# Kernel tuning notes

Measured on AMD Instinct MI355X. Metric: run time of the kernel, lower is better.

The kernel has to match this reference:

```python
import jax, jax.numpy as jnp
import numpy as np

B, TT, T, L, V, E, H = 16, 8, 64, 100, 32000, 512, 512
EO = 2 * H          # encoder output size == decoder hidden size
A = 512             # attention size
IN = E + EO + E     # decoder raw input size
TEMP = IN // 2      # sharp_linear output size
sg = jax.lax.stop_gradient


def _lstm_cell(x, h, c, Wih, Whh, bih, bhh):
    # PyTorch LSTM gate order: i, f, g, o
    g = x @ Wih.T + bih + h @ Whh.T + bhh
    i, f, gg, o = jnp.split(g, 4, axis=-1)
    c = jax.nn.sigmoid(f) * c + jax.nn.sigmoid(i) * jnp.tanh(gg)
    h = jax.nn.sigmoid(o) * jnp.tanh(c)
    return h, c


def setup_inputs():
    key = jax.random.key(0)
    ks = jax.random.split(key, 24)
    s = 0.05
    rn = lambda k, sh: jax.random.normal(k, sh, jnp.float32) * s
    z = lambda *sh: jnp.zeros(sh, jnp.float32)
    return {
        "embedding": rn(ks[0], (V, E)),
        "enc_Wih_f": rn(ks[1], (4 * H, E)), "enc_Whh_f": rn(ks[2], (4 * H, H)),
        "enc_bih_f": z(4 * H), "enc_bhh_f": z(4 * H),
        "enc_Wih_b": rn(ks[3], (4 * H, E)), "enc_Whh_b": rn(ks[4], (4 * H, H)),
        "enc_bih_b": z(4 * H), "enc_bhh_b": z(4 * H),
        "W1": rn(ks[5], (A, EO)), "W2": rn(ks[6], (A, EO)),
        "mem_W": rn(ks[7], (E, EO)), "mem_b": z(E),
        "U1": rn(ks[8], (E, E)), "V1": rn(ks[9], (E, E)),
        "U2": rn(ks[10], (E, E)), "V2": rn(ks[11], (E, E)),
        "sharp_W": rn(ks[12], (TEMP, IN)), "sharp_b": z(TEMP),
        "dec_Wih": rn(ks[13], (4 * EO, TEMP)), "dec_Whh": rn(ks[14], (4 * EO, EO)),
        "dec_bih": z(4 * EO), "dec_bhh": z(4 * EO),
        "fc_W": rn(ks[15], (V, EO)), "fc_b": z(V),
        "topic": jax.random.randint(ks[16], (B, TT), 0, V),
        "topic_len": jnp.full((B,), TT, jnp.int32),
        "essay_input": jax.random.randint(ks[17], (B, T), 0, V),
        "essay_len": jnp.full((B,), T, jnp.int32),
        "mems": jax.random.randint(ks[18], (B, L), 0, V),
    }


def reference(embedding, enc_Wih_f, enc_Whh_f, enc_bih_f, enc_bhh_f,
              enc_Wih_b, enc_Whh_b, enc_bih_b, enc_bhh_b,
              W1, W2, mem_W, mem_b, U1, V1, U2, V2,
              sharp_W, sharp_b, dec_Wih, dec_Whh, dec_bih, dec_bhh,
              fc_W, fc_b, topic, topic_len, essay_input, essay_len, mems):
    Bsz = topic.shape[0]
    Tlen = essay_input.shape[1]

    # ---------------- Encoder (1-layer bidirectional LSTM) ----------------
    # all topic_len equal -> pack/sort is identity
    x = embedding[topic].transpose(1, 0, 2)  # [TT, B, E]

    def mk_cell(Wih, Whh, bih, bhh):
        def f(carry, xt):
            h, c = carry
            h, c = _lstm_cell(xt, h, c, Wih, Whh, bih, bhh)
            return (h, c), h
        return f

    z0 = (jnp.zeros((Bsz, H), x.dtype), jnp.zeros((Bsz, H), x.dtype))
    (hf, cf), outs_f = jax.lax.scan(mk_cell(enc_Wih_f, enc_Whh_f, enc_bih_f, enc_bhh_f), z0, x)
    (hb, cb), outs_b = jax.lax.scan(mk_cell(enc_Wih_b, enc_Whh_b, enc_bih_b, enc_bhh_b), z0, x[::-1])
    outs_b = outs_b[::-1]
    topics = jnp.concatenate([outs_f, outs_b], axis=-1).transpose(1, 0, 2)  # [B, TT, 2H]
    h = jnp.concatenate([hf, hb], axis=-1)  # [B, EO]
    c = jnp.concatenate([cf, cb], axis=-1)  # [B, EO]

    # ---------------- external memory ----------------
    M = embedding[mems]                      # [B, L, E]
    pre_t = topics @ W1.T                    # [B, TT, A]  (precompute attention keys)

    def update_memory(M, emb):
        # all reads of stored memory are detached in the original module
        Md = sg(M)
        e = emb[:, None, :]                  # [B, 1, E]
        Mt = jnp.tanh(Md @ U1.T + e @ V1.T)
        gate = jax.nn.sigmoid(Md @ U2.T + e @ V2.T)
        Mn = gate * Mt + (1.0 - gate) * Md
        return jnp.where(jnp.isfinite(Mn), Mn, jnp.float32(1e-31))

    def before_feed(emb, h_last, c_last, M):
        # topic attention (query = decoder cell state)
        q = c_last @ W2.T                                       # [B, A]
        alpha = jax.nn.softmax(jnp.einsum('bta,ba->bt', pre_t, q), axis=1)
        c_t = jnp.einsum('btd,bt->bd', topics, alpha)           # [B, EO]
        # content-addressed memory read (query = decoder hidden)
        v = jnp.tanh(h_last @ mem_W.T + mem_b)                  # [B, E]
        Md = sg(M)
        qm = jax.nn.softmax(jnp.einsum('ble,be->bl', Md, v), axis=1)
        m_t = jnp.einsum('bl,ble->be', qm, Md)                  # [B, E]
        return jnp.concatenate([emb, c_t, m_t], axis=1)         # [B, IN]

    # ---------------- decode (teacher forcing) ----------------
    emb0 = embedding[essay_input[:, 0]]
    M = update_memory(M, emb0)
    dec_in = before_feed(emb0, h, c, M)

    # steps 1..T-1 feed essay_input[:, t]; last scan step's memory update is unused
    toks = jnp.concatenate([essay_input[:, 1:], essay_input[:, -1:]], axis=1).T  # [T, B]

    def step(carry, tok):
        h, c, M, dec_in = carry
        xs = dec_in @ sharp_W.T + sharp_b
        h, c = _lstm_cell(xs, h, c, dec_Wih, dec_Whh, dec_bih, dec_bhh)
        logits = h @ fc_W.T + fc_b                              # [B, V]
        emb = embedding[tok]
        M = update_memory(M, emb)
        dec_in = before_feed(emb, h, c, M)
        return (h, c, M, dec_in), logits

    _, logits = jax.lax.scan(step, (h, c, M, dec_in), toks)
    return logits.transpose(1, 0, 2)  # [B, T, V]
```

## Files before the change

kernel.cpp:

```cpp
#include <hip/hip_runtime.h>
#include <math.h>

#define DEVI __device__ __forceinline__

typedef unsigned short us8 __attribute__((ext_vector_type(8)));
typedef short bfv __attribute__((ext_vector_type(8)));
typedef float f32x4 __attribute__((ext_vector_type(4)));

DEVI float sigmf_(float x){ return 1.0f/(1.0f+expf(-x)); }
DEVI float dot4_(const float4 a, const float4 b){ return a.x*b.x + a.y*b.y + a.z*b.z + a.w*b.w; }
DEVI float wred64(float v){
#pragma unroll
  for (int m = 32; m; m >>= 1) v += __shfl_xor(v, m);
  return v;
}
DEVI float b2f(unsigned short u){ return __uint_as_float(((unsigned)u)<<16); }
DEVI unsigned short f2bf(float x){
  unsigned u = __float_as_uint(x);
  return (unsigned short)((u + 0x7FFFu + ((u>>16)&1u)) >> 16);
}
DEVI void f2bf2(float x, unsigned short& hi, unsigned short& lo){
  hi = f2bf(x);
  lo = f2bf(x - b2f(hi));
}
// ... 60 lines not shown
}

__global__ void pack_k(const float* __restrict__ U1, const float* __restrict__ U2,
                       const float* __restrict__ sharpW,
                       float* __restrict__ UcatI, float* __restrict__ Ws3T)
{
  int gid = blockIdx.x*256 + threadIdx.x;
  if (gid < 524288){
    int n = gid>>9, k = gid&511;
    UcatI[gid] = (n&1) ? U2[(size_t)(n>>1)*512+k] : U1[(size_t)(n>>1)*512+k];
  } else {
    int g2 = gid - 524288;
    int k = g2>>10, j = g2&1023;
    Ws3T[g2] = sharpW[(size_t)j*2048 + 1536 + k];
  }
}

__global__ void pack_u_hilo(const float* __restrict__ U1, const float* __restrict__ U2,
                            unsigned short* __restrict__ Uhi, unsigned short* __restrict__ Ulo)
{
  int gid = blockIdx.x*256 + threadIdx.x;
  int n = gid>>9, k = gid&511;
  float v = (n&1) ? U2[(size_t)(n>>1)*512+k] : U1[(size_t)(n>>1)*512+k];
  unsigned short h, l;
  f2bf2(v, h, l);
  Uhi[gid] = h; Ulo[gid] = l;
}

__global__ void pack_ws3b(const float* __restrict__ sharpW,
                          unsigned short* __restrict__ hi, unsigned short* __restrict__ lo)
{
  int gid = blockIdx.x*256 + threadIdx.x;
  int j = gid>>9, k = gid&511;
  float v = sharpW[(size_t)j*2048 + 1536 + k];
  unsigned short h, l;
  f2bf2(v, h, l);
  hi[gid] = h; lo[gid] = l;
}

__global__ void conv_k(const float* __restrict__ src, unsigned short* __restrict__ dst, int n8){
  int i = blockIdx.x*256 + threadIdx.x;
  if (i >= n8) return;
  float4 a = ((const float4*)src)[2*i], b = ((const float4*)src)[2*i+1];
  us8 o;
  o[0]=f2bf(a.x); o[1]=f2bf(a.y); o[2]=f2bf(a.z); o[3]=f2bf(a.w);
  o[4]=f2bf(b.x); o[5]=f2bf(b.y); o[6]=f2bf(b.z); o[7]=f2bf(b.w);
  ((us8*)dst)[i] = o;
}

__global__ void conv2_k(const float* __restrict__ src,
                        unsigned short* __restrict__ hi, unsigned short* __restrict__ lo, int n8){
  int i = blockIdx.x*256 + threadIdx.x;
  if (i >= n8) return;
  float4 a = ((const float4*)src)[2*i], b = ((const float4*)src)[2*i+1];
  us8 oh, ol;
  oh[0]=f2bf(a.x); ol[0]=f2bf_lo(a.x, oh[0]);
  oh[1]=f2bf(a.y); ol[1]=f2bf_lo(a.y, oh[1]);
  oh[2]=f2bf(a.z); ol[2]=f2bf_lo(a.z, oh[2]);
  oh[3]=f2bf(a.w); ol[3]=f2bf_lo(a.w, oh[3]);
  oh[4]=f2bf(b.x); ol[4]=f2bf_lo(b.x, oh[4]);
  oh[5]=f2bf(b.y); ol[5]=f2bf_lo(b.y, oh[5]);
  oh[6]=f2bf(b.z); ol[6]=f2bf_lo(b.z, oh[6]);
  oh[7]=f2bf(b.w); ol[7]=f2bf_lo(b.w, oh[7]);
  ((us8*)hi)[i] = oh;
  ((us8*)lo)[i] = ol;
}

template<int ACT>
__global__ void gemm_nt(const float* __restrict__ A, int lda,
                        const float* __restrict__ W, int ldw, int woff,
                        const float* __restrict__ bias,
                        float* __restrict__ C, int ldc, int M, int N, int K)
{
  __shared__ float As[1024], Ws[1024];
  const int bm = blockIdx.y*64, bn = blockIdx.x*64;
  const int tid = threadIdx.x;
  const int lr = tid>>2, lk = (tid&3)<<2;
  const int tm = (tid>>4)<<2, tn = (tid&15)<<2;
  float acc[4][4] = {};
  for (int k0 = 0; k0 < K; k0 += 16){
    float4 av = make_float4(0.f,0.f,0.f,0.f);
    if (bm+lr < M) av = *(const float4*)(A + (size_t)(bm+lr)*lda + k0 + lk);
    As[(lk+0)*64+lr]=av.x; As[(lk+1)*64+lr]=av.y; As[(lk+2)*64+lr]=av.z; As[(lk+3)*64+lr]=av.w;
    float4 wv = make_float4(0.f,0.f,0.f,0.f);
    if (bn+lr < N) wv = *(const float4*)(W + (size_t)(bn+lr)*ldw + woff + k0 + lk);
    Ws[(lk+0)*64+lr]=wv.x; Ws[(lk+1)*64+lr]=wv.y; Ws[(lk+2)*64+lr]=wv.z; Ws[(lk+3)*64+lr]=wv.w;
    __syncthreads();
#pragma unroll
    for (int k = 0; k < 16; ++k){
      float4 a = *(const float4*)&As[k*64+tm];
      float4 w = *(const float4*)&Ws[k*64+tn];
      acc[0][0]+=a.x*w.x; acc[0][1]+=a.x*w.y; acc[0][2]+=a.x*w.z; acc[0][3]+=a.x*w.w;
      acc[1][0]+=a.y*w.x; acc[1][1]+=a.y*w.y; acc[1][2]+=a.y*w.z; acc[1][3]+=a.y*w.w;
      acc[2][0]+=a.z*w.x; acc[2][1]+=a.z*w.y; acc[2][2]+=a.z*w.z; acc[2][3]+=a.z*w.w;
      acc[3][0]+=a.w*w.x; acc[3][1]+=a.w*w.y; acc[3][2]+=a.w*w.z; acc[3][3]+=a.w*w.w;
    }
    __syncthreads();
  }
#pragma unroll
  for (int i = 0; i < 4; ++i){
    int m = bm+tm+i; if (m >= M) continue;
#pragma unroll
    for (int j = 0; j < 4; ++j){
      int n = bn+tn+j; if (n >= N) continue;
      float v = acc[i][j] + (bias ? bias[n] : 0.f);
      if (ACT == 1) v = tanhf(v);
      C[(size_t)m*ldc + n] = v;
    }
  }
}

__global__ void enc_step(const float* __restrict__ xtop,
    const float* __restrict__ Wih_f, const float* __restrict__ Whh_f,
    const float* __restrict__ bih_f, const float* __restrict__ bhh_f,
    const float* __restrict__ Wih_b, const float* __restrict__ Whh_b,
    const float* __restrict__ bih_b, const float* __restrict__ bhh_b,
    const float* __restrict__ h_in, const float* __restrict__ c_in,
    float* __restrict__ h_out, float* __restrict__ c_out,
    float* __restrict__ topics, int t)
{
  const int dir = blockIdx.y;
  const int j = blockIdx.x*4 + (threadIdx.x>>6);
  const int lane = threadIdx.x & 63;
  const int b = lane & 15, g4 = lane >> 4;
  const int tt = dir ? (7 - t) : t;
  const float* Wih = dir ? Wih_b : Wih_f;
  const float* Whh = dir ? Whh_b : Whh_f;
  const float* bih = dir ? bih_b : bih_f;
  const float* bhh = dir ? bhh_b : bhh_f;
  const int row = g4*512 + j;
  float acc = bih[row] + bhh[row];
  const float4* wx = (const float4*)(Wih + (size_t)row*512);
  const float4* xv = (const float4*)(xtop + (size_t)(tt*16+b)*512);
#pragma unroll 8
  for (int k = 0; k < 128; ++k) acc += dot4_(wx[k], xv[k]);
  const float4* wh = (const float4*)(Whh + (size_t)row*512);
  const float4* hv = (const float4*)(h_in + (size_t)b*1024 + dir*512);
#pragma unroll 8
  for (int k = 0; k < 128; ++k) acc += dot4_(wh[k], hv[k]);
  float gi = __shfl(acc, b);
  float gf = __shfl(acc, b+16);
  float gg = __shfl(acc, b+32);
  float go = __shfl(acc, b+48);
  if (g4 == 0){
    float c_old = c_in[(size_t)b*1024 + dir*512 + j];
    float cn = sigmf_(gf)*c_old + sigmf_(gi)*tanhf(gg);
    float hn = sigmf_(go)*tanhf(cn);
    h_out[(size_t)b*1024 + dir*512 + j] = hn;
    c_out[(size_t)b*1024 + dir*512 + j] = cn;
    topics[(size_t)(b*8+tt)*1024 + dir*512 + j] = hn;
  }
}

DEVI void mem_gemm_role(int bid, const float* __restrict__ Min, float* __restrict__ Mout,
                        const float* __restrict__ U,
                        const float* __restrict__ eV1s, const float* __restrict__ eV2s,
                        float* lds, int tid)
{
  const int bm = (bid>>4)*64, bn = (bid&15)*64;
  float* As = lds; float* Ws = lds + 1024;
  const int lr = tid>>2, lk = (tid&3)<<2;
  const int tm = (tid>>4)<<2, tn = (tid&15)<<2;
  float acc[4][4] = {};
  for (int k0 = 0; k0 < 512; k0 += 16){
    float4 av = *(const float4*)(Min + (size_t)(bm+lr)*512 + k0 + lk);
    As[(lk+0)*64+lr]=av.x; As[(lk+1)*64+lr]=av.y; As[(lk+2)*64+lr]=av.z; As[(lk+3)*64+lr]=av.w;
    float4 wv = *(const float4*)(U + (size_t)(bn+lr)*512 + k0 + lk);
    Ws[(lk+0)*64+lr]=wv.x; Ws[(lk+1)*64+lr]=wv.y; Ws[(lk+2)*64+lr]=wv.z; Ws[(lk+3)*64+lr]=wv.w;
    __syncthreads();
#pragma unroll
    for (int k = 0; k < 16; ++k){
      float4 a = *(const float4*)&As[k*64+tm];
      float4 w = *(const float4*)&Ws[k*64+tn];
      acc[0][0]+=a.x*w.x; acc[0][1]+=a.x*w.y; acc[0][2]+=a.x*w.z; acc[0][3]+=a.x*w.w;
      acc[1][0]+=a.y*w.x; acc[1][1]+=a.y*w.y; acc[1][2]+=a.y*w.z; acc[1][3]+=a.y*w.w;
      acc[2][0]+=a.z*w.x; acc[2][1]+=a.z*w.y; acc[2][2]+=a.z*w.z; acc[2][3]+=a.z*w.w;
      acc[3][0]+=a.w*w.x; acc[3][1]+=a.w*w.y; acc[3][2]+=a.w*w.z; acc[3][3]+=a.w*w.w;
    }
    __syncthreads();
  }
  const int e0 = (bn+tn)>>1;
#pragma unroll
  for (int i = 0; i < 4; ++i){
    int r = bm+tm+i;
    int b = r/100;
#pragma unroll
    for (int p = 0; p < 2; ++p){
      int e = e0 + p;
      float oldv = Min[(size_t)r*512 + e];
      float mt = tanhf (acc[i][2*p]   + eV1s[(size_t)b*512 + e]);
      float g  = sigmf_(acc[i][2*p+1] + eV2s[(size_t)b*512 + e]);
      float mn = g*mt + (1.f-g)*oldv;
      if (!isfinite(mn)) mn = 1e-31f;
      Mout[(size_t)r*512 + e] = mn;
    }
  }
}

__global__ void mem_update_k(const float* __restrict__ Min, float* __restrict__ Mout,
                             const float* __restrict__ U,
                             const float* __restrict__ eV1s, const float* __restrict__ eV2s)
{
  __shared__ float lds[2080];
  mem_gemm_role(blockIdx.x, Min, Mout, U, eV1s, eV2s, lds, threadIdx.x);
}

DEVI void mem_ep(f32x4 v, int m0, int n0, int i, int j, int kg, int r16, int lane,
                 const float* __restrict__ Min,
                 const float* __restrict__ eV1s, const float* __restrict__ eV2s,
                 float* __restrict__ Mout,
                 unsigned short* __restrict__ Mohi, unsigned short* __restrict__ Molo)
{
#pragma unroll
  for (int q = 0; q < 4; ++q){
    float val = v[q];
    float oth = __shfl_xor(val, 1);
    if (!(lane&1)){
      int m = m0 + i*16 + kg*4 + q;
      int n = n0 + j*16 + r16;
      int e = n>>1, bb = m/100;
      float mold = Min[(size_t)m*512 + e];
      float mt = tanhf (val + eV1s[(size_t)bb*512 + e]);
      float g  = sigmf_(oth + eV2s[(size_t)bb*512 + e]);
      float mn = g*mt + (1.f-g)*mold;
      if (!isfinite(mn)) mn = 1e-31f;
      Mout[(size_t)m*512 + e] = mn;
      unsigned short h, l;
      f2bf2(mn, h, l);
      Mohi[(size_t)m*512 + e] = h;
      Molo[(size_t)m*512 + e] = l;
    }
  }
}

DEVI void mem_mfma_role2(int hwbid, const float* __restrict__ Min,
                        const unsigned short* __restrict__ Mhi, const unsigned short* __restrict__ Mlo,
                        float* __restrict__ Mout,
                        unsigned short* __restrict__ Mohi, unsigned short* __restrict__ Molo,
                        const unsigned short* __restrict__ Uhi, const unsigned short* __restrict__ Ulo,
                        const float* __restrict__ eV1s, const float* __restrict__ eV2s,
                        int tid, float* __restrict__ lds)
{
  const int bid2 = (hwbid & 7)*200 + (hwbid >> 3);
  const int bm = (bid2 >> 5)*32, bn = (bid2 & 31)*32;
  const int wave = tid>>6, lane = tid&63;
  const int r16 = lane&15, kg = lane>>4;
  const size_t aoff = (size_t)(bm + r16)*512 + wave*128 + kg*8;
  const size_t boff = (size_t)(bn + r16)*512 + wave*128 + kg*8;
  const unsigned short* pa0h = Mhi + aoff; const unsigned short* pa0l = Mlo + aoff;
  const unsigned short* pb0h = Uhi + boff; const unsigned short* pb0l = Ulo + boff;
  f32x4 c00 = {}, c01 = {}, c10 = {}, c11 = {};
#pragma unroll
  for (int k0 = 0; k0 < 128; k0 += 32){
    bfv a0h = *(const bfv*)(pa0h + k0);
    bfv a0l = *(const bfv*)(pa0l + k0);
    bfv a1h = *(const bfv*)(pa0h + 16*512 + k0);
    bfv a1l = *(const bfv*)(pa0l + 16*512 + k0);
    bfv b0h = *(const bfv*)(pb0h + k0);
    bfv b0l = *(const bfv*)(pb0l + k0);
    bfv b1h = *(const bfv*)(pb0h + 16*512 + k0);
    bfv b1l = *(const bfv*)(pb0l + 16*512 + k0);
    c00 = __builtin_amdgcn_mfma_f32_16x16x32_bf16(a0h, b0h, c00, 0, 0, 0);
    c00 = __builtin_amdgcn_mfma_f32_16x16x32_bf16(a0h, b0l, c00, 0, 0, 0);
    c00 = __builtin_amdgcn_mfma_f32_16x16x32_bf16(a0l, b0h, c00, 0, 0, 0);
    c01 = __builtin_amdgcn_mfma_f32_16x16x32_bf16(a0h, b1h, c01, 0, 0, 0);
    c01 = __builtin_amdgcn_mfma_f32_16x16x32_bf16(a0h, b1l, c01, 0, 0, 0);
    c01 = __builtin_amdgcn_mfma_f32_16x16x32_bf16(a0l, b1h, c01, 0, 0, 0);
    c10 = __builtin_amdgcn_mfma_f32_16x16x32_bf16(a1h, b0h, c10, 0, 0, 0);
    c10 = __builtin_amdgcn_mfma_f32_16x16x32_bf16(a1h, b0l, c10, 0, 0, 0);
    c10 = __builtin_amdgcn_mfma_f32_16x16x32_bf16(a1l, b0h, c10, 0, 0, 0);
    c11 = __builtin_amdgcn_mfma_f32_16x16x32_bf16(a1h, b1h, c11, 0, 0, 0);
    c11 = __builtin_amdgcn_mfma_f32_16x16x32_bf16(a1h, b1l, c11, 0, 0, 0);
    c11 = __builtin_amdgcn_mfma_f32_16x16x32_bf16(a1l, b1h, c11, 0, 0, 0);
  }
  float* wbase = lds + wave*1024 + lane*4;
#pragma unroll
  for (int q = 0; q < 4; ++q){
    wbase[q]     = c00[q];
    wbase[256+q] = c01[q];
    wbase[512+q] = c10[q];
    wbase[768+q] = c11[q];
  }
  __syncthreads();
  f32x4 s;
#pragma unroll
  for (int q = 0; q < 4; ++q)
    s[q] = lds[       wave*256 + lane*4 + q] + lds[1024 + wave*256 + lane*4 + q]
         + lds[2048 + wave*256 + lane*4 + q] + lds[3072 + wave*256 + lane*4 + q];
  mem_ep(s, bm, bn, wave>>1, wave&1, kg, r16, lane, Min, eV1s, eV2s, Mout, Mohi, Molo);
}

__global__ __launch_bounds__(256,4) void mem_update_k2(
    const float* __restrict__ Min,
    const unsigned short* __restrict__ Mhi, const unsigned short* __restrict__ Mlo,
    float* __restrict__ Mout,
    unsigned short* __restrict__ Mohi, unsigned short* __restrict__ Molo,
    const unsigned short* __restrict__ Uhi, const unsigned short* __restrict__ Ulo,
    const float* __restrict__ eV1s, const float* __restrict__ eV2s)
{
  __shared__ float lds[4096];
  mem_mfma_role2(blockIdx.x, Min, Mhi, Mlo, Mout, Mohi, Molo, Uhi, Ulo, eV1s, eV2s, threadIdx.x, lds);
}

__global__ void step_pre(const float* __restrict__ Min, float* __restrict__ Mout,
    const float* __restrict__ U,
    const float* __restrict__ eV1s, const float* __restrict__ eV2s,
    const float* __restrict__ qb, const float* __restrict__ vb,
    const float* __restrict__ pret, const float* __restrict__ tws2,
    const float* __restrict__ eWs1t, const float* __restrict__ sharp_b,
    const float* __restrict__ Ws3T, float* __restrict__ xs)
{
  __shared__ float lds[2080];
  const int tid = threadIdx.x;
  if (blockIdx.x >= 16){
    mem_gemm_role(blockIdx.x-16, Min, Mout, U, eV1s, eV2s, lds, tid);
    return;
  }
  const int b = blockIdx.x;
  lds[tid]         = qb[b*512 + tid];
  lds[tid+256]     = qb[b*512 + tid + 256];
  lds[512+tid]     = vb[b*512 + tid];
  lds[512+tid+256] = vb[b*512 + tid + 256];
  __syncthreads();
  {
    const int tq = tid>>5, l32 = tid&31;
    const float* pr = pret + (size_t)(b*8+tq)*512;
    float sv = 0.f;
#pragma unroll
    for (int i = 0; i < 16; ++i){ int a = l32 + 32*i; sv += pr[a]*lds[a]; }
#pragma unroll
    for (int m = 16; m; m >>= 1) sv += __shfl_xor(sv, m);
    if (l32 == 0) lds[1024+tq] = sv;
  }
  __syncthreads();
  {
    float mx = -1e30f;
#pragma unroll
    for (int i = 0; i < 8; ++i) mx = fmaxf(mx, lds[1024+i]);
    float sm = 0.f; float ev[8];
#pragma unroll
    for (int i = 0; i < 8; ++i){ ev[i] = expf(lds[1024+i]-mx); sm += ev[i]; }
    if (tid < 8) lds[1032+tid] = ev[tid]/sm;
  }
  __syncthreads();
  {
    const int wv = tid>>6, lane = tid&63;
    for (int l = wv; l < 100; l += 4){
      const float* Mr = Min + (size_t)(b*100+l)*512;
      float sv = 0.f;
#pragma unroll
      for (int i = 0; i < 8; ++i){ int k = lane + 64*i; sv += Mr[k]*lds[512+k]; }
      sv = wred64(sv);
      if (lane == 0) lds[1040+l] = sv;
    }
  }
  __syncthreads();
  float mx = -1e30f;
  for (int i = 0; i < 100; ++i) mx = fmaxf(mx, lds[1040+i]);
  __syncthreads();
  if (tid < 100) lds[1040+tid] = expf(lds[1040+tid]-mx);
  __syncthreads();
  float sm = 0.f;
  for (int i = 0; i < 100; ++i) sm += lds[1040+i];
  const float inv = 1.f/sm;
  for (int e = tid; e < 512; e += 256){
    float a = 0.f;
    for (int l = 0; l < 100; ++l) a += lds[1040+l]*Min[(size_t)(b*100+l)*512 + e];
    lds[1152+e] = a*inv;
  }
  __syncthreads();
  float a0[4];
#pragma unroll
  for (int r2 = 0; r2 < 4; ++r2){
    int j = tid + 256*r2;
    float v = sharp_b[j] + eWs1t[(size_t)b*1024 + j];
#pragma unroll
    for (int t2 = 0; t2 < 8; ++t2) v += lds[1032+t2]*tws2[(size_t)(b*8+t2)*1024 + j];
    a0[r2] = v;
  }
  for (int k = 0; k < 512; ++k){
    float mk = lds[1152+k];
    const float* wr = Ws3T + (size_t)k*1024;
    a0[0] += mk*wr[tid];
    a0[1] += mk*wr[tid+256];
    a0[2] += mk*wr[tid+512];
    a0[3] += mk*wr[tid+768];
  }
#pragma unroll
  for (int r2 = 0; r2 < 4; ++r2) xs[(size_t)b*1024 + tid + 256*r2] = a0[r2];
}

__global__ __launch_bounds__(256,4) void attn_mt(
    const float* __restrict__ Min,
    const unsigned short* __restrict__ Mhi, const unsigned short* __restrict__ Mlo,
    float* __restrict__ Mout,
    unsigned short* __restrict__ Mohi, unsigned short* __restrict__ Molo,
    const unsigned short* __restrict__ Uhi, const unsigned short* __restrict__ Ulo,
    const float* __restrict__ eV1s, const float* __restrict__ eV2s,
    const float* __restrict__ qb, const float* __restrict__ vb,
    const float* __restrict__ pret,
    float* __restrict__ alphab,
    unsigned short* __restrict__ mthi, unsigned short* __restrict__ mtlo)
{
  __shared__ float lds[4096];
  const int tid = threadIdx.x;
  if (blockIdx.x >= 128){
    mem_mfma_role2(blockIdx.x-128, Min, Mhi, Mlo, Mout, Mohi, Molo, Uhi, Ulo, eV1s, eV2s, tid, lds);
    return;
  }
  const int b = blockIdx.x >> 3, ec = blockIdx.x & 7;
  lds[tid]         = qb[b*512 + tid];
  lds[tid+256]     = qb[b*512 + tid + 256];
  lds[512+tid]     = vb[b*512 + tid];
  lds[512+tid+256] = vb[b*512 + tid + 256];
  __syncthreads();
  if (ec == 0){
    {
      const int tq = tid>>5, l32 = tid&31;
      const float* pr = pret + (size_t)(b*8+tq)*512;
      float sv = 0.f;
#pragma unroll
      for (int i = 0; i < 16; ++i){ int a = l32 + 32*i; sv += pr[a]*lds[a]; }
#pragma unroll
      for (int m = 16; m; m >>= 1) sv += __shfl_xor(sv, m);
      if (l32 == 0) lds[1024+tq] = sv;
    }
    __syncthreads();
    {
      float mx = -1e30f;
#pragma unroll
      for (int i = 0; i < 8; ++i) mx = fmaxf(mx, lds[1024+i]);
      float sm = 0.f; float ev[8];
#pragma unroll
      for (int i = 0; i < 8; ++i){ ev[i] = expf(lds[1024+i]-mx); sm += ev[i]; }
      if (tid < 8) alphab[b*8+tid] = ev[tid]/sm;
    }
    __syncthreads();
  }
  {
    const int wv = tid>>6, lane = tid&63;
    for (int l = wv; l < 100; l += 4){
      const float* Mr = Min + (size_t)(b*100+l)*512;
      float sv = 0.f;
#pragma unroll
      for (int i = 0; i < 8; ++i){ int k = lane + 64*i; sv += Mr[k]*lds[512+k]; }
      sv = wred64(sv);
      if (lane == 0) lds[1040+l] = sv;
    }
  }
  __syncthreads();
  {
    const int wv = tid>>6;
    float v100 = (tid < 100) ? lds[1040+tid] : -1e30f;
    float m1 = v100;
#pragma unroll
    for (int m = 32; m; m >>= 1) m1 = fmaxf(m1, __shfl_xor(m1, m));
    if ((tid&63) == 0) lds[1664+wv] = m1;
    __syncthreads();
    float mx = fmaxf(fmaxf(lds[1664], lds[1665]), fmaxf(lds[1666], lds[1667]));
    float e = (tid < 100) ? expf(v100 - mx) : 0.f;
    float s1 = e;
#pragma unroll
    for (int m = 32; m; m >>= 1) s1 += __shfl_xor(s1, m);
    if ((tid&63) == 0) lds[1668+wv] = s1;
    __syncthreads();
    float sm = lds[1668]+lds[1669]+lds[1670]+lds[1671];
    if (tid < 100) lds[1800+tid] = e/sm;
  }
  __syncthreads();
  {
    const int e = ec*64 + (tid & 63);
    const int lg = tid >> 6;
    float a = 0.f;
    for (int l = lg*25; l < lg*25 + 25; ++l)
      a += lds[1800+l] * Min[(size_t)(b*100 + l)*512 + e];
    lds[1904 + lg*64 + (tid & 63)] = a;
    __syncthreads();
    if (lg == 0){
      float s = lds[1904 + tid] + lds[1968 + tid] + lds[2032 + tid] + lds[2096 + tid];
      unsigned short h, l2;
      f2bf2(s, h, l2);
      mthi[b*512 + e] = h;
      mtlo[b*512 + e] = l2;
    }
  }
}

__global__ __launch_bounds__(256) void xs_k(
    const unsigned short* __restrict__ Ws3hi, const unsigned short* __restrict__ Ws3lo,
    const unsigned short* __restrict__ mthi, const unsigned short* __restrict__ mtlo,
    const float* __restrict__ alphab, const float* __restrict__ sharp_b,
    const float* __restrict__ eWs1t, const float* __restrict__ tws2,
    unsigned short* __restrict__ xshi, unsigned short* __restrict__ xslo)
{
  __shared__ float lds[1024];
  const int tid = threadIdx.x, wave = tid>>6, lane = tid&63;
  const int r16 = lane&15, kg = lane>>4;
  const int jt = blockIdx.x;
  const size_t aoff = (size_t)(jt*16 + r16)*512 + wave*128 + kg*8;
  const size_t boff = (size_t)r16*512 + wave*128 + kg*8;
  f32x4 c0 = {};
#pragma unroll
  for (int k0 = 0; k0 < 128; k0 += 32){
    bfv ah = *(const bfv*)(Ws3hi + aoff + k0);
    bfv al = *(const bfv*)(Ws3lo + aoff + k0);
    bfv bh = *(const bfv*)(mthi + boff + k0);
    bfv bl = *(const bfv*)(mtlo + boff + k0);
    c0 = __builtin_amdgcn_mfma_f32_16x16x32_bf16(ah, bh, c0, 0,0,0);
    c0 = __builtin_amdgcn_mfma_f32_16x16x32_bf16(ah, bl, c0, 0,0,0);
    c0 = __builtin_amdgcn_mfma_f32_16x16x32_bf16(al, bh, c0, 0,0,0);
  }
  float* wb2 = lds + wave*256 + lane*4;
#pragma unroll
  for (int q = 0; q < 4; ++q) wb2[q] = c0[q];
  __syncthreads();
  if (wave == 0){
    const int b = r16;
#pragma unroll
    for (int q = 0; q < 4; ++q){
      float s = lds[lane*4+q] + lds[256+lane*4+q] + lds[512+lane*4+q] + lds[768+lane*4+q];
      int j = jt*16 + kg*4 + q;
      float v2 = s + sharp_b[j] + eWs1t[(size_t)b*1024 + j];
#pragma unroll
      for (int t2 = 0; t2 < 8; ++t2) v2 += alphab[b*8+t2]*tws2[(size_t)(b*8+t2)*1024 + j];
      unsigned short h, l;
      f2bf2(v2, h, l);
      xshi[b*1024+j] = h;
      xslo[b*1024+j] = l;
    }
  }
}

__global__ void dec_lstm(const float* __restrict__ xs,
    const float* __restrict__ Wih, const float* __restrict__ Whh,
    const float* __restrict__ bih, const float* __restrict__ bhh,
    const float* __restrict__ h_in, const float* __restrict__ c_in,
    float* __restrict__ h_out, float* __restrict__ c_out)
{
  const int j = blockIdx.x*4 + (threadIdx.x>>6);
  const int lane = threadIdx.x & 63;
  const int b = lane & 15, g4 = lane >> 4;
  const int row = g4*1024 + j;
  float acc = bih[row] + bhh[row];
  const float4* w1 = (const float4*)(Wih + (size_t)row*1024);
  const float4* x1 = (const float4*)(xs + (size_t)b*1024);
#pragma unroll 8
  for (int k = 0; k < 256; ++k) acc += dot4_(w1[k], x1[k]);
  const float4* w2 = (const float4*)(Whh + (size_t)row*1024);
  const float4* h1 = (const float4*)(h_in + (size_t)b*1024);
#pragma unroll 8
  for (int k = 0; k < 256; ++k) acc += dot4_(w2[k], h1[k]);
  float gi = __shfl(acc, b);
  float gf = __shfl(acc, b+16);
  float gg = __shfl(acc, b+32);
  float go = __shfl(acc, b+48);
  if (g4 == 0){
    float c_old = c_in[(size_t)b*1024 + j];
    float cn = sigmf_(gf)*c_old + sigmf_(gi)*tanhf(gg);
    float hn = sigmf_(go)*tanhf(cn);
    h_out[(size_t)b*1024 + j] = hn;
    c_out[(size_t)b*1024 + j] = cn;
  }
}

__global__ __launch_bounds__(256) void dec_mfma(
    const unsigned short* __restrict__ xsh, const unsigned short* __restrict__ xsl,
    const unsigned short* __restrict__ Wih_h, const unsigned short* __restrict__ Wih_l,
    const unsigned short* __restrict__ Whh_h, const unsigned short* __restrict__ Whh_l,
    const float* __restrict__ bih, const float* __restrict__ bhh,
    const unsigned short* __restrict__ hih, const unsigned short* __restrict__ hil,
    const float* __restrict__ c_in,
    float* __restrict__ h_out, float* __restrict__ c_out,
    unsigned short* __restrict__ hoh, unsigned short* __restrict__ hol,
    unsigned short* __restrict__ coh, unsigned short* __restrict__ col_)
{
  __shared__ float acc_lds[4][4][64][4];
  __shared__ float gat[4][64][4];
  const int tid = threadIdx.x, kh = tid>>6, lane = tid&63;
  const int r16 = lane&15, kg = lane>>4;
  const int jt = blockIdx.x;
  const size_t arow = (size_t)(jt*16 + r16)*1024 + kh*256 + kg*8;
  const size_t boff = (size_t)r16*1024 + kh*256 + kg*8;
  f32x4 c0 = {}, c1 = {}, c2 = {}, c3 = {};
#pragma unroll 2
  for (int k0 = 0; k0 < 256; k0 += 32){
    bfv bxh = *(const bfv*)(xsh + boff + k0);
    bfv bxl = *(const bfv*)(xsl + boff + k0);
    bfv bhh_ = *(const bfv*)(hih + boff + k0);
    bfv bhl_ = *(const bfv*)(hil + boff + k0);
#define DEC_GATE(G, CC) { \
    bfv aih = *(const bfv*)(Wih_h + arow + (size_t)(G)*1048576 + k0); \
    bfv ail = *(const bfv*)(Wih_l + arow + (size_t)(G)*1048576 + k0); \
    bfv ahh = *(const bfv*)(Whh_h + arow + (size_t)(G)*1048576 + k0); \
    bfv ahl = *(const bfv*)(Whh_l + arow + (size_t)(G)*1048576 + k0); \
    CC = __builtin_amdgcn_mfma_f32_16x16x32_bf16(aih, bxh, CC, 0,0,0); \
    CC = __builtin_amdgcn_mfma_f32_16x16x32_bf16(aih, bxl, CC, 0,0,0); \
    CC = __builtin_amdgcn_mfma_f32_16x16x32_bf16(ail, bxh, CC, 0,0,0); \
    CC = __builtin_amdgcn_mfma_f32_16x16x32_bf16(ahh, bhh_, CC, 0,0,0); \
    CC = __builtin_amdgcn_mfma_f32_16x16x32_bf16(ahh, bhl_, CC, 0,0,0); \
    CC = __builtin_amdgcn_mfma_f32_16x16x32_bf16(ahl, bhh_, CC, 0,0,0); }
    DEC_GATE(0, c0)
    DEC_GATE(1, c1)
    DEC_GATE(2, c2)
    DEC_GATE(3, c3)
#undef DEC_GATE
  }
#pragma unroll
  for (int q = 0; q < 4; ++q){
    acc_lds[kh][0][lane][q] = c0[q];
    acc_lds[kh][1][lane][q] = c1[q];
    acc_lds[kh][2][lane][q] = c2[q];
    acc_lds[kh][3][lane][q] = c3[q];
  }
  __syncthreads();
  {
    const int g = kh;
#pragma unroll
    for (int q = 0; q < 4; ++q)
      gat[g][lane][q] = acc_lds[0][g][lane][q] + acc_lds[1][g][lane][q]
                      + acc_lds[2][g][lane][q] + acc_lds[3][g][lane][q];
  }
  __syncthreads();
  {
    const int b = tid&15, joff = tid>>4;
    const int l2 = (joff>>2)*16 + b, q2 = joff&3;
    const int j = jt*16 + joff;
    float gi = gat[0][l2][q2] + bih[j]        + bhh[j];
    float gf = gat[1][l2][q2] + bih[1024+j]   + bhh[1024+j];
    float gg = gat[2][l2][q2] + bih[2048+j]   + bhh[2048+j];
    float go = gat[3][l2][q2] + bih[3072+j]   + bhh[3072+j];
    float cold = c_in[b*1024 + j];
    float cn = sigmf_(gf)*cold + sigmf_(gi)*tanhf(gg);
    float hn = sigmf_(go)*tanhf(cn);
    h_out[b*1024 + j] = hn;
    c_out[b*1024 + j] = cn;
    unsigned short uh, ul;
    f2bf2(hn, uh, ul); hoh[b*1024+j] = uh; hol[b*1024+j] = ul;
    f2bf2(cn, uh, ul); coh[b*1024+j] = uh; col_[b*1024+j] = ul;
  }
}

template<typename WT>
__global__ __launch_bounds__(256,4) void step_out_t(const float* __restrict__ h, const float* __restrict__ c,
    const WT* __restrict__ fcW_, const float* __restrict__ fcb,
    const float* __restrict__ W2, const float* __restrict__ memW,
    const float* __restrict__ memb,
    float* __restrict__ out, float* __restrict__ qb, float* __restrict__ vb, int t)
{
  __shared__ float tile[256];
  const int bid = blockIdx.x;
  const int wv = threadIdx.x>>6, lane = threadIdx.x&63;
  const int b = lane&15, jj = lane>>4;
  if (bid < 2000){
    const int j = bid*16 + wv*4 + jj;
    float acc = kdot1024(fcW_ + (size_t)j*1024, (const float4*)(h + (size_t)b*1024));
    tile[(wv*4+jj)*16 + b] = acc;
    __syncthreads();
    const int b2 = threadIdx.x>>4, j2 = threadIdx.x&15;
    out[(size_t)b2*2048000 + (size_t)t*32000 + bid*16 + j2] = tile[j2*16+b2] + fcb[bid*16+j2];
  } else if (bid < 2032){
    const int j = (bid-2000)*16 + wv*4 + jj;
    float acc = kdot1024(W2 + (size_t)j*1024, (const float4*)(c + (size_t)b*1024));
    qb[b*512 + j] = acc;
  } else {
    const int j = (bid-2032)*16 + wv*4 + jj;
    float acc = kdot1024(memW + (size_t)j*1024, (const float4*)(h + (size_t)b*1024));
    vb[b*512 + j] = tanhf(acc + memb[j]);
  }
}

__global__ __launch_bounds__(256) void step_out_m(
    const unsigned short* __restrict__ fcWb, const float* __restrict__ fcb,
    const unsigned short* __restrict__ W2h, const unsigned short* __restrict__ W2l,
    const unsigned short* __restrict__ mWh, const unsigned short* __restrict__ mWl,
    const float* __restrict__ memb,
    const unsigned short* __restrict__ hh, const unsigned short* __restrict__ hl,
    const unsigned short* __restrict__ ch, const unsigned short* __restrict__ cl,
    float* __restrict__ out, float* __restrict__ qb, float* __restrict__ vb, int t)
{
  const int tid = threadIdx.x, wave = tid>>6, lane = tid&63;
  const int r16 = lane&15, kg = lane>>4;
  const int bid = blockIdx.x;
  const size_t boff = (size_t)r16*1024 + kg*8;
  if (bid < 500){
    const int tile = bid*4 + wave;
    const unsigned short* pa0 = fcWb + (size_t)(tile*16 + r16)*1024 + kg*8;
    const unsigned short* pbh = hh + boff;
    const unsigned short* pbl = hl + boff;
    f32x4 c0 = {};
#pragma unroll 4
    for (int k0 = 0; k0 < 1024; k0 += 32){
      bfv a0 = *(const bfv*)(pa0 + k0);
      bfv b0 = *(const bfv*)(pbh + k0);
      bfv b1 = *(const bfv*)(pbl + k0);
      c0 = __builtin_amdgcn_mfma_f32_16x16x32_bf16(a0, b0, c0, 0,0,0);
      c0 = __builtin_amdgcn_mfma_f32_16x16x32_bf16(a0, b1, c0, 0,0,0);
    }
    float* ob = out + (size_t)r16*2048000 + (size_t)t*32000;
#pragma unroll
    for (int q = 0; q < 4; ++q){
      int j0 = tile*16 + kg*4 + q;
      ob[j0] = c0[q] + fcb[j0];
    }
  } else if (bid < 508){
    const int tile = (bid-500)*4 + wave;
    const unsigned short* pah = W2h + (size_t)(tile*16 + r16)*1024 + kg*8;
    const unsigned short* pal = W2l + (size_t)(tile*16 + r16)*1024 + kg*8;
    const unsigned short* pbh = ch + boff;
    const unsigned short* pbl = cl + boff;
    f32x4 c0 = {};
#pragma unroll 4
    for (int k0 = 0; k0 < 1024; k0 += 32){
      bfv ah = *(const bfv*)(pah + k0);
      bfv al = *(const bfv*)(pal + k0);
      bfv b0 = *(const bfv*)(pbh + k0);
      bfv b1 = *(const bfv*)(pbl + k0);
      c0 = __builtin_amdgcn_mfma_f32_16x16x32_bf16(ah, b0, c0, 0,0,0);
      c0 = __builtin_amdgcn_mfma_f32_16x16x32_bf16(ah, b1, c0, 0,0,0);
      c0 = __builtin_amdgcn_mfma_f32_16x16x32_bf16(al, b0, c0, 0,0,0);
    }
#pragma unroll
    for (int q = 0; q < 4; ++q)
      qb[r16*512 + tile*16 + kg*4 + q] = c0[q];
  } else {
    const int tile = (bid-508)*4 + wave;
    const unsigned short* pah = mWh + (size_t)(tile*16 + r16)*1024 + kg*8;
    const unsigned short* pal = mWl + (size_t)(tile*16 + r16)*1024 + kg*8;
    const unsigned short* pbh = hh + boff;
    const unsigned short* pbl = hl + boff;
    f32x4 c0 = {};
#pragma unroll 4
    for (int k0 = 0; k0 < 1024; k0 += 32){
      bfv ah = *(const bfv*)(pah + k0);
      bfv al = *(const bfv*)(pal + k0);
      bfv b0 = *(const bfv*)(pbh + k0);
      bfv b1 = *(const bfv*)(pbl + k0);
      c0 = __builtin_amdgcn_mfma_f32_16x16x32_bf16(ah, b0, c0, 0,0,0);
      c0 = __builtin_amdgcn_mfma_f32_16x16x32_bf16(ah, b1, c0, 0,0,0);
      c0 = __builtin_amdgcn_mfma_f32_16x16x32_bf16(al, b0, c0, 0,0,0);
    }
#pragma unroll
    for (int q = 0; q < 4; ++q){
      int j = tile*16 + kg*4 + q;
      vb[r16*512 + j] = tanhf(c0[q] + memb[j]);
    }
  }
}

extern "C" void kernel_launch(void* const* d_in, const int* in_sizes, int n_in,
                              void* d_out, int out_size, void* d_ws, size_t ws_size,
                              hipStream_t stream)
{
  const float* embedding = (const float*)d_in[0];
  const float* Wih_f = (const float*)d_in[1];
  const float* Whh_f = (const float*)d_in[2];
  const float* bih_f = (const float*)d_in[3];
  const float* bhh_f = (const float*)d_in[4];
  const float* Wih_b = (const float*)d_in[5];
  const float* Whh_b = (const float*)d_in[6];
  const float* bih_b = (const float*)d_in[7];
  const float* bhh_b = (const float*)d_in[8];
  const float* W1    = (const float*)d_in[9];
  const float* W2    = (const float*)d_in[10];
  const float* mem_W = (const float*)d_in[11];
  const float* mem_b = (const float*)d_in[12];
  const float* U1    = (const float*)d_in[13];
  const float* V1    = (const float*)d_in[14];
  const float* U2    = (const float*)d_in[15];
  const float* V2    = (const float*)d_in[16];
  const float* sharp_W = (const float*)d_in[17];
  const float* sharp_b = (const float*)d_in[18];
  const float* dec_Wih = (const float*)d_in[19];
  const float* dec_Whh = (const float*)d_in[20];
  const float* dec_bih = (const float*)d_in[21];
  const float* dec_bhh = (const float*)d_in[22];
  const float* fc_W  = (const float*)d_in[23];
  const float* fc_b  = (const float*)d_in[24];
  const int* topic   = (const int*)d_in[25];
  const int* essay   = (const int*)d_in[27];
  const int* mems    = (const int*)d_in[29];
  float* out = (float*)d_out;
  float* ws = (float*)d_ws;

  float* x_topic = ws;
  float* embs    = ws + 65536;
  float* eV1     = ws + 598016;
  float* eV2     = ws + 1130496;
  float* eWs1    = ws + 1662976;
  float* topics  = ws + 2727936;
  float* tws2    = ws + 2859008;
  float* pret    = ws + 2990080;
  float* Mb0     = ws + 3055616;
  float* Mb1     = ws + 3874816;
  float* h_buf   = ws + 4694016;
  float* c_buf   = ws + 4726784;
  float* xs      = ws + 4759552;
  float* qb      = ws + 4775936;
  float* vb      = ws + 4784128;
  float* UcatI   = ws + 4792320;
  float* Ws3T    = ws + 5316608;
  unsigned short* Ws3hi = (unsigned short*)(ws + 4792320);
  unsigned short* Ws3lo = (unsigned short*)(ws + 5054464);
  unsigned short* mthi  = (unsigned short*)(ws + 5316608);
  unsigned short* mtlo  = (unsigned short*)(ws + 5320704);
  float*          alphab= ws + 5324800;
  unsigned short* Uhi   = (unsigned short*)(ws + 5840896);
  unsigned short* Ulo   = (unsigned short*)(ws + 6103040);
  unsigned short* Mb0hi = (unsigned short*)(ws + 6365184);
  unsigned short* Mb0lo = (unsigned short*)(ws + 6774784);
  unsigned short* Mb1hi = (unsigned short*)(ws + 7184384);
  unsigned short* Mb1lo = (unsigned short*)(ws + 7593984);
  unsigned short* fcWb  = (unsigned short*)(ws + 8003584);
  unsigned short* dWihHi = (unsigned short*)(ws + 24387584);
  unsigned short* dWihLo = (unsigned short*)(ws + 26484736);
  unsigned short* dWhhHi = (unsigned short*)(ws + 28581888);
  unsigned short* dWhhLo = (unsigned short*)(ws + 30679040);
  unsigned short* W2h    = (unsigned short*)(ws + 32776192);
  unsigned short* W2l    = (unsigned short*)(ws + 33038336);
  unsigned short* mWh    = (unsigned short*)(ws + 33300480);
  unsigned short* mWl    = (unsigned short*)(ws + 33562624);
  unsigned short* hbhi   = (unsigned short*)(ws + 33824768);
  unsigned short* hblo   = (unsigned short*)(ws + 33841152);
  unsigned short* cbhi   = (unsigned short*)(ws + 33857536);
  unsigned short* cblo   = (unsigned short*)(ws + 33873920);
  unsigned short* xshi   = (unsigned short*)(ws + 33890304);
  unsigned short* xslo   = (unsigned short*)(ws + 33898496);

  const size_t NEED2 = (size_t)24387584 * 4;
  const size_t NEED3 = (size_t)33906688 * 4;
  const int tier = (ws_size >= NEED3) ? 3 : (ws_size >= NEED2 ? 2 : 0);

  if (tier < 3){
    zero2_k<<<64,256,0,stream>>>(h_buf, c_buf, 16384);
    gather_k<<<2768,128,0,stream>>>(embedding, topic, essay, mems, x_topic, embs, Mb1, nullptr, nullptr);
    pack_k<<<4096,256,0,stream>>>(U1, U2, sharp_W, UcatI, Ws3T);
    if (tier == 2) conv_k<<<16000,256,0,stream>>>(fc_W, fcWb, 4096000);
    gemm_nt<0><<<dim3(8,17),256,0,stream>>>(embs,512, V1,512,0, nullptr, eV1,512, 1040,512,512);
    gemm_nt<0><<<dim3(8,17),256,0,stream>>>(embs,512, V2,512,0, nullptr, eV2,512, 1040,512,512);
    gemm_nt<0><<<dim3(16,17),256,0,stream>>>(embs,512, sharp_W,2048,0, nullptr, eWs1,1024, 1040,1024,512);
    for (int t = 0; t < 8; ++t){
      const float* hi = h_buf + (t&1)*16384;
      const float* ci = c_buf + (t&1)*16384;
      float* ho = h_buf + ((t+1)&1)*16384;
      float* co = c_buf + ((t+1)&1)*16384;
      enc_step<<<dim3(128,2),256,0,stream>>>(x_topic, Wih_f,Whh_f,bih_f,bhh_f,
                                             Wih_b,Whh_b,bih_b,bhh_b, hi,ci,ho,co, topics, t);
    }
    gemm_nt<0><<<dim3(8,2),256,0,stream>>>(topics,1024, W1,1024,0, nullptr, pret,512, 128,512,1024);
    gemm_nt<0><<<dim3(16,2),256,0,stream>>>(topics,1024, sharp_W,2048,512, nullptr, tws2,1024, 128,1024,1024);
    gemm_nt<0><<<dim3(8,1),256,0,stream>>>(c_buf,1024, W2,1024,0, nullptr, qb,512, 16,512,1024);
    gemm_nt<1><<<dim3(8,1),256,0,stream>>>(h_buf,1024, mem_W,1024,0, mem_b, vb,512, 16,512,1024);
    mem_update_k<<<400,256,0,stream>>>(Mb1, Mb0, UcatI, eV1, eV2);
    for (int t = 0; t < 64; ++t){
      float* Mi = (t&1) ? Mb1 : Mb0;
      float* Mo = (t&1) ? Mb0 : Mb1;
      int nb = (t < 63) ? 416 : 16;
      step_pre<<<nb,256,0,stream>>>(Mi, Mo, UcatI,
          eV1 + (size_t)(t+1)*8192, eV2 + (size_t)(t+1)*8192,
          qb, vb, pret, tws2, eWs1 + (size_t)t*16384, sharp_b, Ws3T, xs);
      const float* hi = h_buf + (t&1)*16384;
      const float* ci = c_buf + (t&1)*16384;
      float* ho = h_buf + ((t+1)&1)*16384;
      float* co = c_buf + ((t+1)&1)*16384;
      dec_lstm<<<256,256,0,stream>>>(xs, dec_Wih, dec_Whh, dec_bih, dec_bhh, hi, ci, ho, co);
      if (tier == 2)
        step_out_t<unsigned short><<<2064,256,0,stream>>>(ho, co, fcWb, fc_b, W2, mem_W, mem_b, out, qb, vb, t);
      else
        step_out_t<float><<<2064,256,0,stream>>>(ho, co, fc_W, fc_b, W2, mem_W, mem_b, out, qb, vb, t);
    }
    return;
  }

  zero2_k<<<64,256,0,stream>>>(h_buf, c_buf, 16384);
  gather_k<<<2768,128,0,stream>>>(embedding, topic, essay, mems, x_topic, embs, Mb1, Mb1hi, Mb1lo);
  pack_u_hilo<<<2048,256,0,stream>>>(U1, U2, Uhi, Ulo);
  pack_ws3b<<<2048,256,0,stream>>>(sharp_W, Ws3hi, Ws3lo);
  conv_k<<<16000,256,0,stream>>>(fc_W, fcWb, 4096000);
  conv2_k<<<2048,256,0,stream>>>(dec_Wih, dWihHi, dWihLo, 524288);
  conv2_k<<<2048,256,0,stream>>>(dec_Whh, dWhhHi, dWhhLo, 524288);
  conv2_k<<<256,256,0,stream>>>(W2, W2h, W2l, 65536);
  conv2_k<<<256,256,0,stream>>>(mem_W, mWh, mWl, 65536);

  gemm_nt<0><<<dim3(8,17),256,0,stream>>>(embs,512, V1,512,0, nullptr, eV1,512, 1040,512,512);
  gemm_nt<0><<<dim3(8,17),256,0,stream>>>(embs,512, V2,512,0, nullptr, eV2,512, 1040,512,512);
  gemm_nt<0><<<dim3(16,17),256,0,stream>>>(embs,512, sharp_W,2048,0, nullptr, eWs1,1024, 1040,1024,512);

  for (int t = 0; t < 8; ++t){
    const float* hi = h_buf + (t&1)*16384;
    const float* ci = c_buf + (t&1)*16384;
    float* ho = h_buf + ((t+1)&1)*16384;
    float* co = c_buf + ((t+1)&1)*16384;
    enc_step<<<dim3(128,2),256,0,stream>>>(x_topic, Wih_f,Whh_f,bih_f,bhh_f,
                                           Wih_b,Whh_b,bih_b,bhh_b, hi,ci,ho,co, topics, t);
  }
  gemm_nt<0><<<dim3(8,2),256,0,stream>>>(topics,1024, W1,1024,0, nullptr, pret,512, 128,512,1024);
  gemm_nt<0><<<dim3(16,2),256,0,stream>>>(topics,1024, sharp_W,2048,512, nullptr, tws2,1024, 128,1024,1024);
  gemm_nt<0><<<dim3(8,1),256,0,stream>>>(c_buf,1024, W2,1024,0, nullptr, qb,512, 16,512,1024);
  gemm_nt<1><<<dim3(8,1),256,0,stream>>>(h_buf,1024, mem_W,1024,0, mem_b, vb,512, 16,512,1024);
  conv2_k<<<8,256,0,stream>>>(h_buf, hbhi, hblo, 2048);
  conv2_k<<<8,256,0,stream>>>(c_buf, cbhi, cblo, 2048);
  mem_update_k2<<<1600,256,0,stream>>>(Mb1, Mb1hi, Mb1lo, Mb0, Mb0hi, Mb0lo, Uhi, Ulo, eV1, eV2);

  for (int t = 0; t < 64; ++t){
    float* Mi = (t&1) ? Mb1 : Mb0;
    unsigned short* Mihi = (t&1) ? Mb1hi : Mb0hi;
    unsigned short* Milo = (t&1) ? Mb1lo : Mb0lo;
    float* Mo = (t&1) ? Mb0 : Mb1;
    unsigned short* Mohi = (t&1) ? Mb0hi : Mb1hi;
    unsigned short* Molo = (t&1) ? Mb0lo : Mb1lo;
    int nb = (t < 63) ? 1728 : 128;
    const int par = t&1, nxt = (t+1)&1;
    attn_mt<<<nb,256,0,stream>>>(Mi, Mihi, Milo, Mo, Mohi, Molo, Uhi, Ulo,
        eV1 + (size_t)(t+1)*8192, eV2 + (size_t)(t+1)*8192,
        qb, vb, pret, alphab, mthi, mtlo);
    xs_k<<<64,256,0,stream>>>(Ws3hi, Ws3lo, mthi, mtlo, alphab, sharp_b,
        eWs1 + (size_t)t*16384, tws2, xshi, xslo);
    const float* ci = c_buf + par*16384;
    float* ho = h_buf + nxt*16384;
    float* co = c_buf + nxt*16384;
    dec_mfma<<<64,256,0,stream>>>(xshi, xslo, dWihHi, dWihLo, dWhhHi, dWhhLo,
        dec_bih, dec_bhh,
        hbhi + par*16384, hblo + par*16384, ci,
        ho, co,
        hbhi + nxt*16384, hblo + nxt*16384, cbhi + nxt*16384, cblo + nxt*16384);
    step_out_m<<<516,256,0,stream>>>(fcWb, fc_b, W2h, W2l, mWh, mWl, mem_b,
        hbhi + nxt*16384, hblo + nxt*16384, cbhi + nxt*16384, cblo + nxt*16384,
        out, qb, vb, t);
  }
}
```

Before: 7.119 ms.

## Defer logits GEMM into next step's attention/memory kernel; split-K q/v projection

The vocabulary logits projection for step t-1 now runs as extra blocks inside the next step's attention-plus-memory-update kernel. This takes it off the serial critical path so it overlaps with the memory-update blocks, and the final step's logits get their own kernel after the loop. The q and v projections that feed attention move into a small separate kernel that splits K across four waves and reduces through LDS, shortening the latency of that dependent step. The cost is a larger fused grid that competes for CUs with the memory-update work, plus an extra kernel launch per step.

```diff
diff --git a/kernel.cpp b/kernel.cpp
--- a/kernel.cpp
+++ b/kernel.cpp
@@ -386,6 +386,42 @@
   mem_mfma_role2(blockIdx.x, Min, Mhi, Mlo, Mout, Mohi, Molo, Uhi, Ulo, eV1s, eV2s, threadIdx.x, lds);
 }
 
+DEVI void logits_role(int lb, int tid,
+    const unsigned short* __restrict__ fcWb, const float* __restrict__ fcb,
+    const unsigned short* __restrict__ hh, const unsigned short* __restrict__ hl,
+    float* __restrict__ out, int t)
+{
+  const int wave = tid>>6, lane = tid&63;
+  const int r16 = lane&15, kg = lane>>4;
+  const int tile = lb*4 + wave;
+  const unsigned short* pa0 = fcWb + (size_t)(tile*16 + r16)*1024 + kg*8;
+  const unsigned short* pbh = hh + (size_t)r16*1024 + kg*8;
+  const unsigned short* pbl = hl + (size_t)r16*1024 + kg*8;
+  f32x4 c0 = {};
+#pragma unroll 4
+  for (int k0 = 0; k0 < 1024; k0 += 32){
+    bfv a0 = *(const bfv*)(pa0 + k0);
+    bfv b0 = *(const bfv*)(pbh + k0);
+    bfv b1 = *(const bfv*)(pbl + k0);
+    c0 = __builtin_amdgcn_mfma_f32_16x16x32_bf16(a0, b0, c0, 0,0,0);
+    c0 = __builtin_amdgcn_mfma_f32_16x16x32_bf16(a0, b1, c0, 0,0,0);
+  }
+  float* ob = out + (size_t)r16*2048000 + (size_t)t*32000;
+#pragma unroll
+  for (int q = 0; q < 4; ++q){
+    int j0 = tile*16 + kg*4 + q;
+    ob[j0] = c0[q] + fcb[j0];
+  }
+}
+
+__global__ __launch_bounds__(256) void logits_k(
+    const unsigned short* __restrict__ fcWb, const float* __restrict__ fcb,
+    const unsigned short* __restrict__ hh, const unsigned short* __restrict__ hl,
+    float* __restrict__ out, int t)
+{
+  logits_role(blockIdx.x, threadIdx.x, fcWb, fcb, hh, hl, out, t);
+}
+
 __global__ void step_pre(const float* __restrict__ Min, float* __restrict__ Mout,
     const float* __restrict__ U,
     const float* __restrict__ eV1s, const float* __restrict__ eV2s,
@@ -474,7 +510,7 @@
   for (int r2 = 0; r2 < 4; ++r2) xs[(size_t)b*1024 + tid + 256*r2] = a0[r2];
 }
 
-__global__ __launch_bounds__(256,4) void attn_mt(
+__global__ __launch_bounds__(256,4) void attn_mega(
     const float* __restrict__ Min,
     const unsigned short* __restrict__ Mhi, const unsigned short* __restrict__ Mlo,
     float* __restrict__ Mout,
@@ -484,12 +520,20 @@
     const float* __restrict__ qb, const float* __restrict__ vb,
     const float* __restrict__ pret,
     float* __restrict__ alphab,
-    unsigned short* __restrict__ mthi, unsigned short* __restrict__ mtlo)
+    unsigned short* __restrict__ mthi, unsigned short* __restrict__ mtlo,
+    const unsigned short* __restrict__ fcWb, const float* __restrict__ fcb,
+    const unsigned short* __restrict__ hph, const unsigned short* __restrict__ hpl,
+    float* __restrict__ out, int tlog, int nLog)
 {
   __shared__ float lds[4096];
   const int tid = threadIdx.x;
   if (blockIdx.x >= 128){
-    mem_mfma_role2(blockIdx.x-128, Min, Mhi, Mlo, Mout, Mohi, Molo, Uhi, Ulo, eV1s, eV2s, tid, lds);
+    const int bid = blockIdx.x - 128;
+    if (bid < nLog){
+      logits_role(bid, tid, fcWb, fcb, hph, hpl, out, tlog);
+      return;
+    }
+    mem_mfma_role2(bid - nLog, Min, Mhi, Mlo, Mout, Mohi, Molo, Uhi, Ulo, eV1s, eV2s, tid, lds);
     return;
   }
   const int b = blockIdx.x >> 3, ec = blockIdx.x & 7;
@@ -724,6 +768,51 @@
   }
 }
 
+__global__ __launch_bounds__(256) void qv_k(
+    const unsigned short* __restrict__ W2h, const unsigned short* __restrict__ W2l,
+    const unsigned short* __restrict__ mWh, const unsigned short* __restrict__ mWl,
+    const float* __restrict__ memb,
+    const unsigned short* __restrict__ hh, const unsigned short* __restrict__ hl,
+    const unsigned short* __restrict__ ch, const unsigned short* __restrict__ cl,
+    float* __restrict__ qb, float* __restrict__ vb)
+{
+  __shared__ float lds[1024];
+  const int tid = threadIdx.x, wave = tid>>6, lane = tid&63;
+  const int r16 = lane&15, kg = lane>>4;
+  const bool isV = blockIdx.x >= 32;
+  const int tile = isV ? ((int)blockIdx.x - 32) : (int)blockIdx.x;
+  const unsigned short* Ah = isV ? mWh : W2h;
+  const unsigned short* Al = isV ? mWl : W2l;
+  const unsigned short* Bh = isV ? hh : ch;
+  const unsigned short* Bl = isV ? hl : cl;
+  const size_t aoff = (size_t)(tile*16 + r16)*1024 + wave*256 + kg*8;
+  const size_t boff = (size_t)r16*1024 + wave*256 + kg*8;
+  f32x4 c0 = {};
+#pragma unroll
+  for (int k0 = 0; k0 < 256; k0 += 32){
+    bfv ah = *(const bfv*)(Ah + aoff + k0);
+    bfv al = *(const bfv*)(Al + aoff + k0);
+    bfv b0 = *(const bfv*)(Bh + boff + k0);
+    bfv b1 = *(const bfv*)(Bl + boff + k0);
+    c0 = __builtin_amdgcn_mfma_f32_16x16x32_bf16(ah, b0, c0, 0,0,0);
+    c0 = __builtin_amdgcn_mfma_f32_16x16x32_bf16(ah, b1, c0, 0,0,0);
+    c0 = __builtin_amdgcn_mfma_f32_16x16x32_bf16(al, b0, c0, 0,0,0);
+  }
+  float* wb2 = lds + wave*256 + lane*4;
+#pragma unroll
+  for (int q = 0; q < 4; ++q) wb2[q] = c0[q];
+  __syncthreads();
+  if (wave == 0){
+#pragma unroll
+    for (int q = 0; q < 4; ++q){
+      float s = lds[lane*4+q] + lds[256+lane*4+q] + lds[512+lane*4+q] + lds[768+lane*4+q];
+      int j = tile*16 + kg*4 + q;
+      if (isV) vb[r16*512 + j] = tanhf(s + memb[j]);
+      else     qb[r16*512 + j] = s;
+    }
+  }
+}
+
 template<typename WT>
 __global__ __launch_bounds__(256,4) void step_out_t(const float* __restrict__ h, const float* __restrict__ c,
     const WT* __restrict__ fcW_, const float* __restrict__ fcb,
@@ -750,84 +839,6 @@
     const int j = (bid-2032)*16 + wv*4 + jj;
     float acc = kdot1024(memW + (size_t)j*1024, (const float4*)(h + (size_t)b*1024));
     vb[b*512 + j] = tanhf(acc + memb[j]);
-  }
-}
-
-__global__ __launch_bounds__(256) void step_out_m(
-    const unsigned short* __restrict__ fcWb, const float* __restrict__ fcb,
-    const unsigned short* __restrict__ W2h, const unsigned short* __restrict__ W2l,
-    const unsigned short* __restrict__ mWh, const unsigned short* __restrict__ mWl,
-    const float* __restrict__ memb,
-    const unsigned short* __restrict__ hh, const unsigned short* __restrict__ hl,
-    const unsigned short* __restrict__ ch, const unsigned short* __restrict__ cl,
-    float* __restrict__ out, float* __restrict__ qb, float* __restrict__ vb, int t)
-{
-  const int tid = threadIdx.x, wave = tid>>6, lane = tid&63;
-  const int r16 = lane&15, kg = lane>>4;
-  const int bid = blockIdx.x;
-  const size_t boff = (size_t)r16*1024 + kg*8;
-  if (bid < 500){
-    const int tile = bid*4 + wave;
-    const unsigned short* pa0 = fcWb + (size_t)(tile*16 + r16)*1024 + kg*8;
-    const unsigned short* pbh = hh + boff;
-    const unsigned short* pbl = hl + boff;
-    f32x4 c0 = {};
-#pragma unroll 4
-    for (int k0 = 0; k0 < 1024; k0 += 32){
-      bfv a0 = *(const bfv*)(pa0 + k0);
-      bfv b0 = *(const bfv*)(pbh + k0);
-      bfv b1 = *(const bfv*)(pbl + k0);
-      c0 = __builtin_amdgcn_mfma_f32_16x16x32_bf16(a0, b0, c0, 0,0,0);
-      c0 = __builtin_amdgcn_mfma_f32_16x16x32_bf16(a0, b1, c0, 0,0,0);
-    }
-    float* ob = out + (size_t)r16*2048000 + (size_t)t*32000;
-#pragma unroll
-    for (int q = 0; q < 4; ++q){
-      int j0 = tile*16 + kg*4 + q;
-      ob[j0] = c0[q] + fcb[j0];
-    }
-  } else if (bid < 508){
-    const int tile = (bid-500)*4 + wave;
-    const unsigned short* pah = W2h + (size_t)(tile*16 + r16)*1024 + kg*8;
-    const unsigned short* pal = W2l + (size_t)(tile*16 + r16)*1024 + kg*8;
-    const unsigned short* pbh = ch + boff;
-    const unsigned short* pbl = cl + boff;
-    f32x4 c0 = {};
-#pragma unroll 4
-    for (int k0 = 0; k0 < 1024; k0 += 32){
-      bfv ah = *(const bfv*)(pah + k0);
-      bfv al = *(const bfv*)(pal + k0);
-      bfv b0 = *(const bfv*)(pbh + k0);
-      bfv b1 = *(const bfv*)(pbl + k0);
-      c0 = __builtin_amdgcn_mfma_f32_16x16x32_bf16(ah, b0, c0, 0,0,0);
-      c0 = __builtin_amdgcn_mfma_f32_16x16x32_bf16(ah, b1, c0, 0,0,0);
-      c0 = __builtin_amdgcn_mfma_f32_16x16x32_bf16(al, b0, c0, 0,0,0);
-    }
-#pragma unroll
-    for (int q = 0; q < 4; ++q)
-      qb[r16*512 + tile*16 + kg*4 + q] = c0[q];
-  } else {
-    const int tile = (bid-508)*4 + wave;
-    const unsigned short* pah = mWh + (size_t)(tile*16 + r16)*1024 + kg*8;
-    const unsigned short* pal = mWl + (size_t)(tile*16 + r16)*1024 + kg*8;
-    const unsigned short* pbh = hh + boff;
-    const unsigned short* pbl = hl + boff;
-    f32x4 c0 = {};
-#pragma unroll 4
-    for (int k0 = 0; k0 < 1024; k0 += 32){
-      bfv ah = *(const bfv*)(pah + k0);
-      bfv al = *(const bfv*)(pal + k0);
-      bfv b0 = *(const bfv*)(pbh + k0);
-      bfv b1 = *(const bfv*)(pbl + k0);
-      c0 = __builtin_amdgcn_mfma_f32_16x16x32_bf16(ah, b0, c0, 0,0,0);
-      c0 = __builtin_amdgcn_mfma_f32_16x16x32_bf16(ah, b1, c0, 0,0,0);
-      c0 = __builtin_amdgcn_mfma_f32_16x16x32_bf16(al, b0, c0, 0,0,0);
-    }
-#pragma unroll
-    for (int q = 0; q < 4; ++q){
-      int j = tile*16 + kg*4 + q;
-      vb[r16*512 + j] = tanhf(c0[q] + memb[j]);
-    }
   }
 }
 
@@ -992,11 +1003,13 @@
     float* Mo = (t&1) ? Mb0 : Mb1;
     unsigned short* Mohi = (t&1) ? Mb0hi : Mb1hi;
     unsigned short* Molo = (t&1) ? Mb0lo : Mb1lo;
-    int nb = (t < 63) ? 1728 : 128;
     const int par = t&1, nxt = (t+1)&1;
-    attn_mt<<<nb,256,0,stream>>>(Mi, Mihi, Milo, Mo, Mohi, Molo, Uhi, Ulo,
+    const int nLog = (t > 0) ? 500 : 0;
+    const int nGemm = (t < 63) ? 1600 : 0;
+    attn_mega<<<128 + nLog + nGemm,256,0,stream>>>(Mi, Mihi, Milo, Mo, Mohi, Molo, Uhi, Ulo,
         eV1 + (size_t)(t+1)*8192, eV2 + (size_t)(t+1)*8192,
-        qb, vb, pret, alphab, mthi, mtlo);
+        qb, vb, pret, alphab, mthi, mtlo,
+        fcWb, fc_b, hbhi + par*16384, hblo + par*16384, out, t-1, nLog);
     xs_k<<<64,256,0,stream>>>(Ws3hi, Ws3lo, mthi, mtlo, alphab, sharp_b,
         eWs1 + (size_t)t*16384, tws2, xshi, xslo);
     const float* ci = c_buf + par*16384;
@@ -1007,8 +1020,9 @@
         hbhi + par*16384, hblo + par*16384, ci,
         ho, co,
         hbhi + nxt*16384, hblo + nxt*16384, cbhi + nxt*16384, cblo + nxt*16384);
-    step_out_m<<<516,256,0,stream>>>(fcWb, fc_b, W2h, W2l, mWh, mWl, mem_b,
-        hbhi + nxt*16384, hblo + nxt*16384, cbhi + nxt*16384, cblo + nxt*16384,
-        out, qb, vb, t);
-  }
-}
+    if (t < 63)
+      qv_k<<<64,256,0,stream>>>(W2h, W2l, mWh, mWl, mem_b,
+          hbhi + nxt*16384, hblo + nxt*16384, cbhi + nxt*16384, cblo + nxt*16384, qb, vb);
+  }
+  logits_k<<<500,256,0,stream>>>(fcWb, fc_b, hbhi, hblo, out, 63);
+}
```

New measurement: 6.817 ms, median of 2. -4.2%, faster.
